# Kernel tuning notes

Hardware: AMD Instinct MI355X
Metric: run time of the kernel (lower is better)

## Reference

```python
import jax, jax.numpy as jnp
import numpy as np

D_MODEL = 1024
NHEAD = 16
HEAD_DIM = D_MODEL // NHEAD
LN_EPS = 1e-5


def _retention_scan(v, lam_h):
    # v: (B, L, H, DH); lam_h: (H,)
    # recurrence: s_0 = v_0; s_t = lam * s_{t-1} + v_t
    B, L, H, DH = v.shape
    a = jnp.broadcast_to(lam_h[None, None, :, None], v.shape)

    def combine(x, y):
        a1, b1 = x
        a2, b2 = y
        return (a1 * a2, a2 * b1 + b2)

    _, states = jax.lax.associative_scan(combine, (a, v), axis=1)
    return states


def setup_inputs() -> dict:
    key = jax.random.key(0)
    ks = jax.random.split(key, 6)
    B, L, D = 4, 4096, D_MODEL
    s = 1.0 / np.sqrt(D)
    return {
        "x": jax.random.normal(ks[0], (B, L, D), jnp.float32),
        "Wq": jax.random.normal(ks[1], (D, D), jnp.float32) * s,
        "Wv": jax.random.normal(ks[2], (D, D), jnp.float32) * s,
        "Wg": jax.random.normal(ks[3], (D, D), jnp.float32) * s,
        "Wo": jax.random.normal(ks[4], (D, D), jnp.float32) * s,
        "beta": jnp.full((NHEAD,), -0.2, jnp.float32),
        "ln_gamma": jnp.ones((D_MODEL,), jnp.float32),
        "ln_beta": jnp.zeros((D_MODEL,), jnp.float32),
    }


def reference(x, Wq, Wv, Wg, Wo, beta, ln_gamma, ln_beta):
    B, L, D = x.shape
    H, DH = NHEAD, HEAD_DIM
    # projections (torch Linear: x @ W.T)
    q = (x @ Wq.T).reshape(B, L, H, DH)
    v = (x @ Wv.T).reshape(B, L, H, DH)
    lam_h = jax.nn.sigmoid(beta)
    state = _retention_scan(v, lam_h)  # (B, L, H, DH)
    y = (q * state).reshape(B, L, D)
    # LayerNorm over last dim
    mu = jnp.mean(y, axis=-1, keepdims=True)
    var = jnp.mean((y - mu) ** 2, axis=-1, keepdims=True)
    y = (y - mu) * jax.lax.rsqrt(var + LN_EPS) * ln_gamma + ln_beta
    # SiLU gate
    gate = jax.nn.silu(x @ Wg.T)
    y = y * gate
    return y @ Wo.T
```

## Files before the change

kernel.cpp:

```cpp
#include <hip/hip_runtime.h>

#define BB 4
#define LL 4096
#define DM 1024
#define NH 16
#define MM (BB * LL)
#define CC2 256
#define LC2 16

#define BKT 64
#define NKT (DM / BKT)

typedef unsigned short u16;
typedef float f32x4 __attribute__((ext_vector_type(4)));
typedef int i32x4 __attribute__((ext_vector_type(4)));
typedef __bf16 mfma_in __attribute__((ext_vector_type(8)));

__device__ __forceinline__ u16 f2bf(float f) {
    unsigned u = __float_as_uint(f);
    u += 0x7FFFu + ((u >> 16) & 1u);
    return (u16)(u >> 16);
}
__device__ __forceinline__ float bf2f(u16 u) {
    return __uint_as_float(((unsigned)u) << 16);
}

__device__ __forceinline__ void gld_lds16(const u16* g, u16* l) {
    __builtin_amdgcn_global_load_lds(
        (const __attribute__((address_space(1))) void*)g,
        (__attribute__((address_space(3))) void*)l,
        16, 0, 0);
}

__device__ __forceinline__ mfma_in ds_read128(const u16* p) {
    i32x4 r;
    unsigned off = (unsigned)(size_t)(const __attribute__((address_space(3))) u16*)p;
    asm volatile("ds_read_b128 %0, %1" : "=v"(r) : "v"(off));
    return __builtin_bit_cast(mfma_in, r);
}

#define XF4 (MM * DM / 4)
#define WF4 (DM * DM / 4)
__global__ __launch_bounds__(256)
void cvt_all(const float* __restrict__ x,
             const float* __restrict__ w0, const float* __restrict__ w1,
             const float* __restrict__ w2, const float* __restrict__ w3,
             u16* __restrict__ dst) {
    int i = blockIdx.x * 256 + threadIdx.x;
    const float* src;
    int si;
    if (i < XF4) { src = x; si = i; }
    else {
        int j = i - XF4;
        int w = j >> 18;
        si = j & (WF4 - 1);
        src = (w == 0) ? w0 : (w == 1) ? w1 : (w == 2) ? w2 : w3;
    }
    float4 f = ((const float4*)src)[si];
    ushort4 o;
    o.x = f2bf(f.x); o.y = f2bf(f.y); o.z = f2bf(f.z); o.w = f2bf(f.w);
    ((ushort4*)dst)[i] = o;
}


template<int IOFF, int JOFF>
__device__ __forceinline__ void mfma8(const mfma_in (&a)[4], const mfma_in (&b)[2],
                                      f32x4 (&acc)[8][4]) {
#pragma unroll
    for (int i = 0; i < 4; i++)
#pragma unroll
        for (int j = 0; j < 2; j++)
            acc[IOFF + i][JOFF + j] = __builtin_amdgcn_mfma_f32_16x16x32_bf16(
                a[i], b[j], acc[IOFF + i][JOFF + j], 0, 0, 0);
}

#define WAITL(n) do { \
    asm volatile("s_waitcnt lgkmcnt(" #n ")"); \
    __builtin_amdgcn_sched_barrier(0); \
} while (0)

__device__ __forceinline__ void mainloop256(
    const u16* __restrict__ A, const u16* __restrict__ B,
    int mBlk, int nBlk,
    u16 (*__restrict__ As)[256 * 64], u16 (*__restrict__ Bs)[256 * 64],
    f32x4 (&acc)[8][4]) {
    const int tid  = threadIdx.x;
    const int wave = tid >> 6;
    const int lane = tid & 63;
    const int quad = lane >> 4;
    const int l16  = lane & 15;
    const int wm   = (wave >> 2) * 128;
    const int wn   = (wave & 3) * 64;

    const int sRow = wave * 8 + (lane >> 3);
    const int sCol = ((lane & 7) ^ (lane >> 3)) * 8;
    const u16* gA = A + (size_t)(mBlk + sRow) * DM + sCol;
    const u16* gB = B + (size_t)(nBlk + sRow) * DM + sCol;
    const int ldsW = wave * 8 * 64;

    int rA[8], rB[4];
#pragma unroll
    for (int i = 0; i < 8; i++) rA[i] = (wm + i * 16 + l16) * 64;
#pragma unroll
    for (int j = 0; j < 4; j++) rB[j] = (wn + j * 16 + l16) * 64;
    const int c0 = ((quad    ) ^ (l16 & 7)) * 8;
    const int c1 = ((quad + 4) ^ (l16 & 7)) * 8;

#define STG4_A(dst, t) do { \
    const int kk_ = ((t) & (NKT - 1)) * BKT; \
    gld_lds16(gA + kk_,                   (dst) + ldsW); \
    gld_lds16(gA + (size_t) 64 * DM + kk_, (dst) +  64 * 64 + ldsW); \
    gld_lds16(gA + (size_t)128 * DM + kk_, (dst) + 128 * 64 + ldsW); \
    gld_lds16(gA + (size_t)192 * DM + kk_, (dst) + 192 * 64 + ldsW); \
} while (0)
#define STG4_B(dst, t) do { \
    const int kk_ = ((t) & (NKT - 1)) * BKT; \
    gld_lds16(gB + kk_,                   (dst) + ldsW); \
    gld_lds16(gB + (size_t) 64 * DM + kk_, (dst) +  64 * 64 + ldsW); \
    gld_lds16(gB + (size_t)128 * DM + kk_, (dst) + 128 * 64 + ldsW); \
    gld_lds16(gB + (size_t)192 * DM + kk_, (dst) + 192 * 64 + ldsW); \
} while (0)
#define RDA(dst, idx, cc) (dst) = ds_read128(curA + rA[idx] + (cc))
#define RDB(dst, idx, cc) (dst) = ds_read128(curB + rB[idx] + (cc))

    mfma_in aLs0[4], aHs0[4], bLs0[2], bHs0[2];
    mfma_in aLs1[4], aHs1[4], bLs1[2], bHs1[2];

    STG4_A(As[0], 0);
    STG4_B(Bs[0], 0);
    asm volatile("s_waitcnt vmcnt(0)");
    __builtin_amdgcn_s_barrier();

#pragma unroll 1
    for (int kt = 0; kt < NKT; ++kt) {
        const int cur = kt & 1, nxt = cur ^ 1;
        const u16* curA = As[cur];
        const u16* curB = Bs[cur];

#pragma unroll
        for (int i = 0; i < 4; i++) RDA(aLs0[i], i, c0);
#pragma unroll
        for (int j = 0; j < 2; j++) RDB(bLs0[j], j, c0);
#pragma unroll
        for (int i = 0; i < 4; i++) RDA(aHs0[i], i + 4, c0);
        STG4_A(As[nxt], kt + 1);
        __builtin_amdgcn_sched_barrier(0);

        WAITL(4);
        __builtin_amdgcn_s_setprio(1);
        mfma8<0, 0>(aLs0, bLs0, acc);
        __builtin_amdgcn_s_setprio(0);

#pragma unroll
        for (int j = 0; j < 2; j++) RDB(bHs0[j], j + 2, c0);
        WAITL(2);
        __builtin_amdgcn_s_setprio(1);
        mfma8<4, 0>(aHs0, bLs0, acc);
        __builtin_amdgcn_s_setprio(0);

#pragma unroll
        for (int i = 0; i < 4; i++) RDA(aLs1[i], i, c1);
        WAITL(4);
        __builtin_amdgcn_s_setprio(1);
        mfma8<0, 2>(aLs0, bHs0, acc);
        mfma8<4, 2>(aHs0, bHs0, acc);
        __builtin_amdgcn_s_setprio(0);

#pragma unroll
        for (int j = 0; j < 2; j++) RDB(bLs1[j], j, c1);
#pragma unroll
        for (int i = 0; i < 4; i++) RDA(aHs1[i], i + 4, c1);
        STG4_B(Bs[nxt], kt + 1);
        __builtin_amdgcn_sched_barrier(0);

        WAITL(4);
        __builtin_amdgcn_s_setprio(1);
        mfma8<0, 0>(aLs1, bLs1, acc);
        __builtin_amdgcn_s_setprio(0);

#pragma unroll
        for (int j = 0; j < 2; j++) RDB(bHs1[j], j + 2, c1);
        WAITL(2);
        __builtin_amdgcn_s_setprio(1);
        mfma8<4, 0>(aHs1, bLs1, acc);
        __builtin_amdgcn_s_setprio(0);

        WAITL(0);
        __builtin_amdgcn_s_setprio(1);
        mfma8<0, 2>(aLs1, bHs1, acc);
        mfma8<4, 2>(aHs1, bHs1, acc);
        __builtin_amdgcn_s_setprio(0);

        __builtin_amdgcn_sched_barrier(0);
        asm volatile("s_waitcnt vmcnt(0)");
        __builtin_amdgcn_sched_barrier(0);
        __builtin_amdgcn_s_barrier();
    }
#undef STG4_A
#undef STG4_B
#undef RDA
#undef RDB
}

__global__ __launch_bounds__(512, 2)
void gemm_qvg(const u16* __restrict__ A, const u16* __restrict__ B,
              u16* __restrict__ oq, u16* __restrict__ ov, u16* __restrict__ og,
              const float* __restrict__ beta, float* __restrict__ ebuf) {
    __shared__ __align__(16) u16 As[2][256 * 64];
    __shared__ __align__(16) u16 Bs[2][256 * 64];
    const int mBlk = blockIdx.x * 256;
    const int nBlk = blockIdx.y * 256;

    f32x4 acc[8][4] = {};
    mainloop256(A, B, mBlk, nBlk, As, Bs, acc);

    const int tid  = threadIdx.x;
    const int wave = tid >> 6;
    const int lane = tid & 63;
    const int quad = lane >> 4;
    const int l16  = lane & 15;
    const int wm   = (wave >> 2) * 128;
    const int wn   = (wave & 3) * 64;

    u16* outs[3] = {oq, ov, og};
    u16* O = outs[nBlk >> 10];
    const int nIn = nBlk & 1023;
#pragma unroll
    for (int i = 0; i < 8; i++) {
        int row0 = mBlk + wm + i * 16 + quad * 4;
#pragma unroll
        for (int j = 0; j < 4; j++) {
            int col = nIn + wn + j * 16 + l16;
#pragma unroll
            for (int r = 0; r < 4; r++)
                O[(size_t)(row0 + r) * DM + col] = f2bf(acc[i][j][r]);
        }
    }

    if ((nBlk >> 10) == 1) {
        const int rowB = mBlk + wm;
        const int b    = rowB >> 12;
        const int cB   = (rowB & 4095) >> 4;
#pragma unroll
        for (int j = 0; j < 4; j++) {
            int col = nIn + wn + j * 16 + l16;
            float lam  = 1.0f / (1.0f + __expf(-beta[col >> 6]));
            float lam2 = lam * lam, lam4 = lam2 * lam2, lam8 = lam4 * lam4;
            float w = quad == 0 ? lam4 * lam8 : quad == 1 ? lam8
                    : quad == 2 ? lam4 : 1.0f;
#pragma unroll
            for (int i = 0; i < 8; i++) {
                f32x4 a = acc[i][j];
                float p = ((a[0] * lam + a[1]) * lam + a[2]) * lam + a[3];
                float v = p * w;
                v += __shfl_xor(v, 16);
                v += __shfl_xor(v, 32);
                if (quad == 0)
                    ebuf[((size_t)b * CC2 + (cB + i)) * DM + col] = v;
            }
        }
    }
}

__global__ __launch_bounds__(512, 2)
void gemm_out(const u16* __restrict__ A, const u16* __restrict__ B,
              float* __restrict__ C) {
    __shared__ __align__(16) u16 As[2][256 * 64];
    __shared__ __align__(16) u16 Bs[2][256 * 64];
    const int mBlk = blockIdx.x * 256;
    const int nBlk = blockIdx.y * 256;

    f32x4 acc[8][4] = {};
    mainloop256(A, B, mBlk, nBlk, As, Bs, acc);

    const int tid  = threadIdx.x;
    const int wave = tid >> 6;
    const int lane = tid & 63;
    const int quad = lane >> 4;
    const int l16  = lane & 15;
    const int wm   = (wave >> 2) * 128;
    const int wn   = (wave & 3) * 64;

#pragma unroll
    for (int i = 0; i < 8; i++) {
        int row0 = mBlk + wm + i * 16 + quad * 4;
#pragma unroll
        for (int j = 0; j < 4; j++) {
            int col = nBlk + wn + j * 16 + l16;
#pragma unroll
            for (int r = 0; r < 4; r++)
                C[(size_t)(row0 + r) * DM + col] = acc[i][j][r];
        }
    }
}

__global__ __launch_bounds__(256)
void scan_carry(const float* __restrict__ ebuf, const float* __restrict__ beta,
                float* __restrict__ carry) {
    int ch = blockIdx.x * 256 + threadIdx.x;
    int b = ch >> 10, d = ch & 1023;
    int h = d >> 6;
    float lam = 1.0f / (1.0f + __expf(-beta[h]));
    float lamC = lam;
    for (int i = 0; i < 4; i++) lamC *= lamC;
    float cur = 0.0f;
#pragma unroll 8
    for (int c = 0; c < CC2; c++) {
        size_t idx = ((size_t)b * CC2 + c) * DM + d;
        carry[idx] = cur;
        cur = lamC * cur + ebuf[idx];
    }
}

__global__ __launch_bounds__(256)
void scan_ln_gate(const u16* __restrict__ v, const u16* __restrict__ q,
                  const u16* __restrict__ g, const float* __restrict__ carry,
                  const float* __restrict__ beta, const float* __restrict__ gamma,
                  const float* __restrict__ lnb, u16* __restrict__ out) {
    __shared__ float red[2][8];
    const int t = threadIdx.x;
    const int c = blockIdx.x, b = blockIdx.y;
    const int wave = t >> 6, lane = t & 63;
    const int d0 = t * 4;
    const int h = d0 >> 6;
    float lam = 1.0f / (1.0f + __expf(-beta[h]));
    float4 gm = ((const float4*)gamma)[t];
    float4 bt = ((const float4*)lnb)[t];
    float4 cr = *(const float4*)(carry + ((size_t)b * CC2 + c) * DM + d0);
    float s0 = cr.x, s1 = cr.y, s2 = cr.z, s3 = cr.w;
    size_t base = ((size_t)b * LL + (size_t)c * LC2) * DM + d0;

    for (int i = 0; i < LC2; i++) {
        ushort4 v4 = *(const ushort4*)(v + base);
        ushort4 q4 = *(const ushort4*)(q + base);
        ushort4 g4 = *(const ushort4*)(g + base);
        s0 = lam * s0 + bf2f(v4.x);
        s1 = lam * s1 + bf2f(v4.y);
        s2 = lam * s2 + bf2f(v4.z);
        s3 = lam * s3 + bf2f(v4.w);
        float y0 = bf2f(q4.x) * s0, y1 = bf2f(q4.y) * s1;
        float y2 = bf2f(q4.z) * s2, y3 = bf2f(q4.w) * s3;
        float sum = y0 + y1 + y2 + y3;
        float sq  = y0 * y0 + y1 * y1 + y2 * y2 + y3 * y3;
#pragma unroll
        for (int off = 32; off > 0; off >>= 1) {
            sum += __shfl_xor(sum, off);
            sq  += __shfl_xor(sq, off);
        }
        int p = i & 1;
        if (lane == 0) { red[p][wave] = sum; red[p][4 + wave] = sq; }
        __syncthreads();
        float ts = red[p][0] + red[p][1] + red[p][2] + red[p][3];
        float tq = red[p][4] + red[p][5] + red[p][6] + red[p][7];
        float mu  = ts * (1.0f / DM);
        float inv = rsqrtf(tq * (1.0f / DM) - mu * mu + 1e-5f);

        float gv0 = bf2f(g4.x), gv1 = bf2f(g4.y), gv2 = bf2f(g4.z), gv3 = bf2f(g4.w);
        float x0 = ((y0 - mu) * inv * gm.x + bt.x) * (gv0 / (1.0f + __expf(-gv0)));
        float x1 = ((y1 - mu) * inv * gm.y + bt.y) * (gv1 / (1.0f + __expf(-gv1)));
        float x2 = ((y2 - mu) * inv * gm.z + bt.z) * (gv2 / (1.0f + __expf(-gv2)));
        float x3 = ((y3 - mu) * inv * gm.w + bt.w) * (gv3 / (1.0f + __expf(-gv3)));
        ushort4 o;
        o.x = f2bf(x0); o.y = f2bf(x1); o.z = f2bf(x2); o.w = f2bf(x3);
        *(ushort4*)(out + base) = o;
        base += DM;
    }
}

extern "C" void kernel_launch(void* const* d_in, const int* in_sizes, int n_in,
                              void* d_out, int out_size, void* d_ws, size_t ws_size,
                              hipStream_t stream) {
    const float* x     = (const float*)d_in[0];
    const float* Wq    = (const float*)d_in[1];
    const float* Wv    = (const float*)d_in[2];
    const float* Wg    = (const float*)d_in[3];
    const float* Wo    = (const float*)d_in[4];
    const float* beta  = (const float*)d_in[5];
    const float* gamma = (const float*)d_in[6];
    const float* lnb   = (const float*)d_in[7];

    u16* xb  = (u16*)d_ws;
    u16* Wqb = xb + (size_t)MM * DM;
    u16* Wob = Wqb + (size_t)3 * DM * DM;
    u16* qb  = Wob + (size_t)DM * DM;
    u16* vb  = qb + (size_t)MM * DM;
    u16* gb  = vb + (size_t)MM * DM;
    float* ebuf  = (float*)(gb + (size_t)MM * DM);
    float* carry = ebuf + (size_t)BB * CC2 * DM;
    u16* yfin = xb;

    cvt_all<<<(XF4 + 4 * WF4 + 255) / 256, 256, 0, stream>>>(x, Wq, Wv, Wg, Wo, xb);

    dim3 gq(MM / 256, 3 * DM / 256);
    gemm_qvg<<<gq, 512, 0, stream>>>(xb, Wqb, qb, vb, gb, beta, ebuf);

    scan_carry<<<(BB * DM) / 256, 256, 0, stream>>>(ebuf, beta, carry);
    dim3 gf(CC2, BB);
    scan_ln_gate<<<gf, 256, 0, stream>>>(vb, qb, gb, carry, beta, gamma, lnb, yfin);

    dim3 go(MM / 256, DM / 256);
    gemm_out<<<go, 512, 0, stream>>>(yfin, Wob, (float*)d_out);
}
```

Before: 316.0 us.

## Map one wave per row chunk in scan_ln_gate and skip redundant last-tile prefetch

Result: slower. 322.4 us (+2.0%).

```diff
diff --git a/kernel.cpp b/kernel.cpp
--- a/kernel.cpp
+++ b/kernel.cpp
@@ -107,15 +107,15 @@
     const int c1 = ((quad + 4) ^ (l16 & 7)) * 8;
 
 #define STG4_A(dst, t) do { \
-    const int kk_ = ((t) & (NKT - 1)) * BKT; \
-    gld_lds16(gA + kk_,                   (dst) + ldsW); \
+    const int kk_ = (t) * BKT; \
+    gld_lds16(gA + kk_,                    (dst) + ldsW); \
     gld_lds16(gA + (size_t) 64 * DM + kk_, (dst) +  64 * 64 + ldsW); \
     gld_lds16(gA + (size_t)128 * DM + kk_, (dst) + 128 * 64 + ldsW); \
     gld_lds16(gA + (size_t)192 * DM + kk_, (dst) + 192 * 64 + ldsW); \
 } while (0)
 #define STG4_B(dst, t) do { \
-    const int kk_ = ((t) & (NKT - 1)) * BKT; \
-    gld_lds16(gB + kk_,                   (dst) + ldsW); \
+    const int kk_ = (t) * BKT; \
+    gld_lds16(gB + kk_,                    (dst) + ldsW); \
     gld_lds16(gB + (size_t) 64 * DM + kk_, (dst) +  64 * 64 + ldsW); \
     gld_lds16(gB + (size_t)128 * DM + kk_, (dst) + 128 * 64 + ldsW); \
     gld_lds16(gB + (size_t)192 * DM + kk_, (dst) + 192 * 64 + ldsW); \
@@ -136,6 +136,7 @@
         const int cur = kt & 1, nxt = cur ^ 1;
         const u16* curA = As[cur];
         const u16* curB = Bs[cur];
+        const bool pre = (kt + 1 < NKT);
 
 #pragma unroll
         for (int i = 0; i < 4; i++) RDA(aLs0[i], i, c0);
@@ -143,7 +144,7 @@
         for (int j = 0; j < 2; j++) RDB(bLs0[j], j, c0);
 #pragma unroll
         for (int i = 0; i < 4; i++) RDA(aHs0[i], i + 4, c0);
-        STG4_A(As[nxt], kt + 1);
+        if (pre) STG4_A(As[nxt], kt + 1);
         __builtin_amdgcn_sched_barrier(0);
 
         WAITL(4);
@@ -170,7 +171,7 @@
         for (int j = 0; j < 2; j++) RDB(bLs1[j], j, c1);
 #pragma unroll
         for (int i = 0; i < 4; i++) RDA(aHs1[i], i + 4, c1);
-        STG4_B(Bs[nxt], kt + 1);
+        if (pre) STG4_B(Bs[nxt], kt + 1);
         __builtin_amdgcn_sched_barrier(0);
 
         WAITL(4);
@@ -317,52 +318,64 @@
                   const u16* __restrict__ g, const float* __restrict__ carry,
                   const float* __restrict__ beta, const float* __restrict__ gamma,
                   const float* __restrict__ lnb, u16* __restrict__ out) {
-    __shared__ float red[2][8];
     const int t = threadIdx.x;
-    const int c = blockIdx.x, b = blockIdx.y;
     const int wave = t >> 6, lane = t & 63;
-    const int d0 = t * 4;
-    const int h = d0 >> 6;
-    float lam = 1.0f / (1.0f + __expf(-beta[h]));
-    float4 gm = ((const float4*)gamma)[t];
-    float4 bt = ((const float4*)lnb)[t];
-    float4 cr = *(const float4*)(carry + ((size_t)b * CC2 + c) * DM + d0);
-    float s0 = cr.x, s1 = cr.y, s2 = cr.z, s3 = cr.w;
+    const int c = blockIdx.x * 4 + wave;
+    const int b = blockIdx.y;
+    const int d0 = lane * 16;
+    float lam = 1.0f / (1.0f + __expf(-beta[d0 >> 6]));
+
+    float s[16], gm[16], bt[16];
+    {
+        const float4* cp = (const float4*)(carry + ((size_t)b * CC2 + c) * DM + d0);
+        const float4* gp = (const float4*)(gamma + d0);
+        const float4* bp = (const float4*)(lnb + d0);
+#pragma unroll
+        for (int k = 0; k < 4; k++) {
+            float4 cv = cp[k], gv = gp[k], bv = bp[k];
+            s[4*k+0] = cv.x; s[4*k+1] = cv.y; s[4*k+2] = cv.z; s[4*k+3] = cv.w;
+            gm[4*k+0] = gv.x; gm[4*k+1] = gv.y; gm[4*k+2] = gv.z; gm[4*k+3] = gv.w;
+            bt[4*k+0] = bv.x; bt[4*k+1] = bv.y; bt[4*k+2] = bv.z; bt[4*k+3] = bv.w;
+        }
+    }
+
     size_t base = ((size_t)b * LL + (size_t)c * LC2) * DM + d0;
-
+#pragma unroll 1
     for (int i = 0; i < LC2; i++) {
-        ushort4 v4 = *(const ushort4*)(v + base);
-        ushort4 q4 = *(const ushort4*)(q + base);
-        ushort4 g4 = *(const ushort4*)(g + base);
-        s0 = lam * s0 + bf2f(v4.x);
-        s1 = lam * s1 + bf2f(v4.y);
-        s2 = lam * s2 + bf2f(v4.z);
-        s3 = lam * s3 + bf2f(v4.w);
-        float y0 = bf2f(q4.x) * s0, y1 = bf2f(q4.y) * s1;
-        float y2 = bf2f(q4.z) * s2, y3 = bf2f(q4.w) * s3;
-        float sum = y0 + y1 + y2 + y3;
-        float sq  = y0 * y0 + y1 * y1 + y2 * y2 + y3 * y3;
+        float y[16];
+        float sum = 0.0f, sq = 0.0f;
+#pragma unroll
+        for (int k = 0; k < 4; k++) {
+            ushort4 vv = ((const ushort4*)(v + base))[k];
+            ushort4 qq = ((const ushort4*)(q + base))[k];
+            float s0 = (s[4*k+0] = lam * s[4*k+0] + bf2f(vv.x));
+            float s1 = (s[4*k+1] = lam * s[4*k+1] + bf2f(vv.y));
+            float s2 = (s[4*k+2] = lam * s[4*k+2] + bf2f(vv.z));
+            float s3 = (s[4*k+3] = lam * s[4*k+3] + bf2f(vv.w));
+            float y0 = bf2f(qq.x) * s0, y1 = bf2f(qq.y) * s1;
+            float y2 = bf2f(qq.z) * s2, y3 = bf2f(qq.w) * s3;
+            y[4*k+0] = y0; y[4*k+1] = y1; y[4*k+2] = y2; y[4*k+3] = y3;
+            sum += (y0 + y1) + (y2 + y3);
+            sq  += (y0 * y0 + y1 * y1) + (y2 * y2 + y3 * y3);
+        }
 #pragma unroll
         for (int off = 32; off > 0; off >>= 1) {
             sum += __shfl_xor(sum, off);
             sq  += __shfl_xor(sq, off);
         }
-        int p = i & 1;
-        if (lane == 0) { red[p][wave] = sum; red[p][4 + wave] = sq; }
-        __syncthreads();
-        float ts = red[p][0] + red[p][1] + red[p][2] + red[p][3];
-        float tq = red[p][4] + red[p][5] + red[p][6] + red[p][7];
-        float mu  = ts * (1.0f / DM);
-        float inv = rsqrtf(tq * (1.0f / DM) - mu * mu + 1e-5f);
-
-        float gv0 = bf2f(g4.x), gv1 = bf2f(g4.y), gv2 = bf2f(g4.z), gv3 = bf2f(g4.w);
-        float x0 = ((y0 - mu) * inv * gm.x + bt.x) * (gv0 / (1.0f + __expf(-gv0)));
-        float x1 = ((y1 - mu) * inv * gm.y + bt.y) * (gv1 / (1.0f + __expf(-gv1)));
-        float x2 = ((y2 - mu) * inv * gm.z + bt.z) * (gv2 / (1.0f + __expf(-gv2)));
-        float x3 = ((y3 - mu) * inv * gm.w + bt.w) * (gv3 / (1.0f + __expf(-gv3)));
-        ushort4 o;
-        o.x = f2bf(x0); o.y = f2bf(x1); o.z = f2bf(x2); o.w = f2bf(x3);
-        *(ushort4*)(out + base) = o;
+        float mu  = sum * (1.0f / DM);
+        float inv = rsqrtf(sq * (1.0f / DM) - mu * mu + 1e-5f);
+#pragma unroll
+        for (int k = 0; k < 4; k++) {
+            ushort4 gg = ((const ushort4*)(g + base))[k];
+            float g0 = bf2f(gg.x), g1 = bf2f(gg.y), g2 = bf2f(gg.z), g3 = bf2f(gg.w);
+            ushort4 o;
+            o.x = f2bf(((y[4*k+0] - mu) * inv * gm[4*k+0] + bt[4*k+0]) * (g0 / (1.0f + __expf(-g0))));
+            o.y = f2bf(((y[4*k+1] - mu) * inv * gm[4*k+1] + bt[4*k+1]) * (g1 / (1.0f + __expf(-g1))));
+            o.z = f2bf(((y[4*k+2] - mu) * inv * gm[4*k+2] + bt[4*k+2]) * (g2 / (1.0f + __expf(-g2))));
+            o.w = f2bf(((y[4*k+3] - mu) * inv * gm[4*k+3] + bt[4*k+3]) * (g3 / (1.0f + __expf(-g3))));
+            ((ushort4*)(out + base))[k] = o;
+        }
         base += DM;
     }
 }
@@ -395,7 +408,7 @@
     gemm_qvg<<<gq, 512, 0, stream>>>(xb, Wqb, qb, vb, gb, beta, ebuf);
 
     scan_carry<<<(BB * DM) / 256, 256, 0, stream>>>(ebuf, beta, carry);
-    dim3 gf(CC2, BB);
+    dim3 gf(CC2 / 4, BB);
     scan_ln_gate<<<gf, 256, 0, stream>>>(vb, qb, gb, carry, beta, gamma, lnb, yfin);
 
     dim3 go(MM / 256, DM / 256);
```
